# Kernel optimization log

Measured on AMD Instinct MI355X. Metric: run time of the kernel, lower is better.

The kernel has to match this reference:

```python
import jax, jax.numpy as jnp
import numpy as np

B, S, D, H, L, FF = 32, 512, 256, 8, 2, 512
E = 64  # embed_dim_per_feature
VOCABS = [20, 50, 100]
NCLS = 36
MAX_CONN, THR = 10, 0.6


def _ln(x, g, b, eps=1e-5):
    m = x.mean(-1, keepdims=True)
    v = ((x - m) ** 2).mean(-1, keepdims=True)
    return g * (x - m) / jnp.sqrt(v + eps) + b


def _build_adj(cat, cnt):
    # self loops + chain links + banded similarity links (create_mutation_graph_optimized)
    Bb, _, Ss = cat.shape
    adj = jnp.broadcast_to(jnp.eye(Ss, dtype=jnp.float32), (Bb, Ss, Ss))
    for d in range(1, MAX_CONN):
        if d >= Ss:
            break
        cat_sim = (cat[:, :, :-d] == cat[:, :, d:]).astype(jnp.float32).mean(1)
        cnt_sim = jnp.exp(-jnp.abs(cnt[:, :-d] - cnt[:, d:]) / 100.0)
        sim = 0.5 * (cat_sim + cnt_sim)  # [B, S-d]
        base = 1.0 if d == 1 else 0.0  # chain link stays 1 when sim<=thr
        val = jnp.where(sim > THR, sim, base)
        ii = jnp.arange(Ss - d)
        adj = adj.at[:, ii, ii + d].set(val)
        adj = adj.at[:, ii + d, ii].set(val)
    return adj


def setup_inputs():
    key = jax.random.key(0)
    ks = iter(jax.random.split(key, 40))
    def nrm(shape, s=0.02):
        return jax.random.normal(next(ks), shape, jnp.float32) * s
    return {
        "categorical_x": jax.random.randint(next(ks), (B, 3, S), 0, min(VOCABS)),
        "count_x": jax.random.uniform(next(ks), (B, S), jnp.float32) * 100.0,
        "emb0": nrm((VOCABS[0], E)), "emb1": nrm((VOCABS[1], E)), "emb2": nrm((VOCABS[2], E)),
        "cnt_W": nrm((1, E)), "cnt_b": jnp.zeros((E,), jnp.float32),
        "pos_enc": nrm((S, D)),
        "gat_W": nrm((L, D, D)), "gat_a": nrm((L, 2 * D, 1)),
        "qkv_W": nrm((L, 3 * D, D)), "qkv_b": jnp.zeros((L, 3 * D), jnp.float32),
        "outp_W": nrm((L, D, D)), "outp_b": jnp.zeros((L, D), jnp.float32),
        "ff1_W": nrm((L, FF, D)), "ff1_b": jnp.zeros((L, FF), jnp.float32),
        "ff2_W": nrm((L, D, FF)), "ff2_b": jnp.zeros((L, D), jnp.float32),
        "ln_g": jnp.ones((L, 3, D), jnp.float32), "ln_b": jnp.zeros((L, 3, D), jnp.float32),
        "cls1_W": nrm((D // 2, D)), "cls1_b": jnp.zeros((D // 2,), jnp.float32),
        "cls2_W": nrm((NCLS, D // 2)), "cls2_b": jnp.zeros((NCLS,), jnp.float32),
    }


def reference(categorical_x, count_x, emb0, emb1, emb2, cnt_W, cnt_b, pos_enc,
              gat_W, gat_a, qkv_W, qkv_b, outp_W, outp_b,
              ff1_W, ff1_b, ff2_W, ff2_b, ln_g, ln_b,
              cls1_W, cls1_b, cls2_W, cls2_b):
    Ss = categorical_x.shape[2]
    # per-timestep feature embedding + count projection, concat -> d_model
    x = jnp.concatenate([
        emb0[categorical_x[:, 0]], emb1[categorical_x[:, 1]], emb2[categorical_x[:, 2]],
        count_x[..., None] @ cnt_W + cnt_b], -1)
    x = x + pos_enc[:Ss]
    mask = _build_adj(categorical_x, count_x) > 0  # adj used only as mask
    dh = D // H
    for l in range(L):
        # GraphAttentionLayer: e_ij = Wh_i.a1 + Wh_j.a2 (same math as repeat+concat+matmul)
        Wh = x @ gat_W[l]
        e = (Wh @ gat_a[l][:D, 0])[:, :, None] + (Wh @ gat_a[l][D:, 0])[:, None, :]
        att = jax.nn.softmax(jnp.where(mask, e, -9e15), -1)
        g = jax.nn.elu(att @ Wh)
        x = _ln(x + g, ln_g[l, 0], ln_b[l, 0])
        # MultiheadAttention (batch_first, eval)
        qkv = x @ qkv_W[l].T + qkv_b[l]
        q, k, v = jnp.split(qkv, 3, -1)
        q = q.reshape(-1, Ss, H, dh)
        k = k.reshape(-1, Ss, H, dh)
        v = v.reshape(-1, Ss, H, dh)
        sc = jnp.einsum('bihd,bjhd->bhij', q, k) / jnp.sqrt(jnp.float32(dh))
        o = jnp.einsum('bhij,bjhd->bihd', jax.nn.softmax(sc, -1), v).reshape(-1, Ss, D)
        o = o @ outp_W[l].T + outp_b[l]
        x = _ln(x + o, ln_g[l, 1], ln_b[l, 1])
        # FFN
        ff = jax.nn.relu(x @ ff1_W[l].T + ff1_b[l]) @ ff2_W[l].T + ff2_b[l]
        x = _ln(x + ff, ln_g[l, 2], ln_b[l, 2])
    pooled = x.mean(1)
    h = jax.nn.relu(pooled @ cls1_W.T + cls1_b)
    return h @ cls2_W.T + cls2_b
```

## Files before the change

kernel.cpp:

```cpp
#include <hip/hip_runtime.h>
#include <hip/hip_bf16.h>
#include <math.h>

#define Bn 32
#define Sn 512
#define Dn 256
#define Hn 8
#define DHn 32
#define En 64
#define FFn 512
#define Ln 2
#define NCLSn 36
#define BANDR 9
#define NBn 19
#define Mn (Bn * Sn)

typedef __attribute__((ext_vector_type(8))) short s8v;
typedef __attribute__((ext_vector_type(4))) float f4v;
typedef __attribute__((ext_vector_type(4))) unsigned short us4;
typedef unsigned short ushortT;

__device__ __forceinline__ ushortT f2b(float f) {
    unsigned u = __float_as_uint(f);
    unsigned r = (u + 0x7FFFu + ((u >> 16) & 1u)) >> 16;
    return (ushortT)r;
}

#define GLDS16(g, l)                                                            \
    __builtin_amdgcn_global_load_lds(                                           \
        (const __attribute__((address_space(1))) void*)(g),                     \
        (__attribute__((address_space(3))) void*)(l), 16, 0, 0)

__global__ void k_f2b_all(const float* __restrict__ qkvW, const float* __restrict__ outpW,
                          const float* __restrict__ ff1W, const float* __restrict__ ff2W,
                          const float* __restrict__ gatW,
                          ushortT* __restrict__ qkvWb, ushortT* __restrict__ outpWb,
                          ushortT* __restrict__ ff1Wb, ushortT* __restrict__ ff2Wb,
                          ushortT* __restrict__ gatWb) {
    int bid = blockIdx.x;
    if (bid < 1024) {
        int i4 = bid * 256 + threadIdx.x;
        const float* src; ushortT* dst; int off;
        if (i4 < 98304)       { src = qkvW;  dst = qkvWb;  off = 0; }
        else if (i4 < 131072) { src = outpW; dst = outpWb; off = 98304; }
        else if (i4 < 196608) { src = ff1W;  dst = ff1Wb;  off = 131072; }
        else                  { src = ff2W;  dst = ff2Wb;  off = 196608; }
        int j = (i4 - off) * 4;
        float4 v = *(const float4*)(src + j);
        us4 o = {f2b(v.x), f2b(v.y), f2b(v.z), f2b(v.w)};
        *(us4*)(dst + j) = o;
    } else {
        int i = (bid - 1024) * 256 + threadIdx.x;
        int l = i >> 16, rem = i & 65535;
        int k = rem >> 8, n = rem & 255;
        gatWb[(l << 16) + n * 256 + k] = f2b(gatW[i]);
    }
}

__global__ void k_embed_mask(const int* __restrict__ cat, const float* __restrict__ cnt,
                             const float* __restrict__ e0, const float* __restrict__ e1,
                             const float* __restrict__ e2,
                             const float* __restrict__ cW, const float* __restrict__ cb,
                             const float* __restrict__ pos, float* __restrict__ x,
                             ushortT* __restrict__ xb, unsigned char* __restrict__ maskp) {
    if (blockIdx.x < Mn) {
        int bs = blockIdx.x;
        int d = threadIdx.x;
        int b = bs >> 9, s = bs & 511;
        float v;
        if (d < 64)       v = e0[cat[(b * 3 + 0) * Sn + s] * En + d];
        else if (d < 128) v = e1[cat[(b * 3 + 1) * Sn + s] * En + (d - 64)];
        else if (d < 192) v = e2[cat[(b * 3 + 2) * Sn + s] * En + (d - 128)];
        else              v = cnt[b * Sn + s] * cW[d - 192] + cb[d - 192];
        float y = v + pos[s * Dn + d];
        x[(size_t)bs * Dn + d] = y;
        xb[(size_t)bs * Dn + d] = f2b(y);
    } else {
        int idx = (blockIdx.x - Mn) * 256 + threadIdx.x;
        if (idx >= Bn * Sn * NBn) return;
        int off = idx % NBn;
        int bs = idx / NBn;
        int b = bs >> 9, i = bs & 511;
        int j = i + off - BANDR;
        unsigned char m = 0;
        if (j >= 0 && j < Sn) {
            int dd = off - BANDR;
            int ad = dd < 0 ? -dd : dd;
            if (ad <= 1) {
                m = 1;
            } else {
                int c = 0;
                for (int f = 0; f < 3; f++)
                    c += (cat[(b * 3 + f) * Sn + i] == cat[(b * 3 + f) * Sn + j]);
                float cat_sim = (float)c / 3.0f;
                float cnt_sim = expf(-fabsf(cnt[b * Sn + i] - cnt[b * Sn + j]) / 100.0f);
                float sim = 0.5f * (cat_sim + cnt_sim);
                m = (sim > 0.6f) ? 1 : 0;
            }
        }
        maskp[idx] = m;
    }
}

template <int ACT>
__global__ __launch_bounds__(256) void k_gemm_mfma(const ushortT* __restrict__ A,
                                                   const ushortT* __restrict__ Bt,
                                                   const float* __restrict__ bias,
                                                   ushortT* __restrict__ Cout,
                                                   int M, int N, int K) {
    __shared__ ushortT As[2][128 * 32];
    __shared__ ushortT Bs[2][128 * 32];
    int tid = threadIdx.x;
    int w = tid >> 6, lane = tid & 63;
    int g = lane >> 4, lr = lane & 15;
    int m0 = blockIdx.y * 128, n0 = blockIdx.x * 128;
    int wr = w >> 1, wc = w & 1;
    int NT = K >> 5;
    f4v acc[4][4];
#pragma unroll
    for (int m = 0; m < 4; m++)
#pragma unroll
        for (int n = 0; n < 4; n++) acc[m][n] = (f4v){0.f, 0.f, 0.f, 0.f};

    auto stage = [&](int t, int buf) {
        int k0 = t << 5;
#pragma unroll
        for (int r = 0; r < 2; r++) {
            int e = (tid + r * 256) * 8;
            int row = e >> 5, kk = e & 31;
            GLDS16(A + (size_t)(m0 + row) * K + k0 + kk, &As[buf][e]);
            GLDS16(Bt + (size_t)(n0 + row) * K + k0 + kk, &Bs[buf][e]);
        }
    };

    stage(0, 0);
    __syncthreads();
    for (int t = 0; t < NT; t++) {
        int cur = t & 1;
        if (t + 1 < NT) stage(t + 1, cur ^ 1);
        s8v af[4], bf[4];
#pragma unroll
        for (int m = 0; m < 4; m++)
            af[m] = *(const s8v*)(&As[cur][(wr * 64 + m * 16 + lr) * 32 + g * 8]);
#pragma unroll
        for (int n = 0; n < 4; n++)
            bf[n] = *(const s8v*)(&Bs[cur][(wc * 64 + n * 16 + lr) * 32 + g * 8]);
#pragma unroll
        for (int m = 0; m < 4; m++)
#pragma unroll
            for (int n = 0; n < 4; n++)
                acc[m][n] = __builtin_amdgcn_mfma_f32_16x16x32_bf16(af[m], bf[n], acc[m][n], 0, 0, 0);
        __syncthreads();
    }
#pragma unroll
    for (int m = 0; m < 4; m++) {
#pragma unroll
        for (int n = 0; n < 4; n++) {
            int col = n0 + wc * 64 + n * 16 + lr;
            float bv = bias ? bias[col] : 0.0f;
#pragma unroll
            for (int r = 0; r < 4; r++) {
                int row = m0 + wr * 64 + m * 16 + g * 4 + r;
                float v = acc[m][n][r] + bv;
                if (ACT == 1) v = fmaxf(v, 0.0f);
                Cout[(size_t)row * N + col] = f2b(v);
            }
        }
    }
}

template <int MODE>
__global__ __launch_bounds__(256) void k_gemm_row(const ushortT* __restrict__ A,
                                                  const ushortT* __restrict__ Bt,
                                                  const float* __restrict__ bias,
                                                  const float* __restrict__ ga,
                                                  float* __restrict__ a1h, float* __restrict__ a2h,
                                                  float* __restrict__ Whout,
                                                  const float* __restrict__ lg,
                                                  const float* __restrict__ lb,
                                                  float* __restrict__ x, ushortT* __restrict__ xb,
                                                  int K) {
    __shared__ ushortT As[2][32 * 32];
    __shared__ ushortT Bs[2][256 * 32];
    __shared__ float red1[32][4], red2[32][4];
    int tid = threadIdx.x;
    int w = tid >> 6, lane = tid & 63;
    int g = lane >> 4, lr = lane & 15;
    int m0 = blockIdx.x * 32;
    int NT = K >> 5;
    f4v acc[2][4];
#pragma unroll
    for (int m = 0; m < 2; m++)
#pragma unroll
        for (int n = 0; n < 4; n++) acc[m][n] = (f4v){0.f, 0.f, 0.f, 0.f};

    auto stage = [&](int t, int buf) {
        int k0 = t << 5;
        if (tid < 128) {
            int e = tid * 8;
            int row = e >> 5, kk = e & 31;
            GLDS16(A + (size_t)(m0 + row) * K + k0 + kk, &As[buf][e]);
        }
#pragma unroll
        for (int r = 0; r < 4; r++) {
            int e = (tid + r * 256) * 8;
            int row = e >> 5, kk = e & 31;
            GLDS16(Bt + (size_t)row * K + k0 + kk, &Bs[buf][e]);
        }
    };

    stage(0, 0);
    __syncthreads();
    for (int t = 0; t < NT; t++) {
        int cur = t & 1;
        if (t + 1 < NT) stage(t + 1, cur ^ 1);
        s8v af[2], bf[4];
#pragma unroll
        for (int m = 0; m < 2; m++)
            af[m] = *(const s8v*)(&As[cur][(m * 16 + lr) * 32 + g * 8]);
#pragma unroll
        for (int n = 0; n < 4; n++)
            bf[n] = *(const s8v*)(&Bs[cur][(w * 64 + n * 16 + lr) * 32 + g * 8]);
#pragma unroll
        for (int m = 0; m < 2; m++)
#pragma unroll
            for (int n = 0; n < 4; n++)
                acc[m][n] = __builtin_amdgcn_mfma_f32_16x16x32_bf16(af[m], bf[n], acc[m][n], 0, 0, 0);
        __syncthreads();
    }

    int cn[4];
#pragma unroll
    for (int n = 0; n < 4; n++) cn[n] = w * 64 + n * 16 + lr;

    if constexpr (MODE == 0) {
        float a1v[4], a2v[4];
#pragma unroll
        for (int n = 0; n < 4; n++) { a1v[n] = ga[cn[n]]; a2v[n] = ga[Dn + cn[n]]; }
#pragma unroll
        for (int m = 0; m < 2; m++)
#pragma unroll
            for (int r = 0; r < 4; r++) {
                int rowl = m * 16 + g * 4 + r;
                float p1 = 0.f, p2 = 0.f;
#pragma unroll
                for (int n = 0; n < 4; n++) {
                    float v = acc[m][n][r];
                    Whout[(size_t)(m0 + rowl) * Dn + cn[n]] = v;
                    p1 += v * a1v[n];
                    p2 += v * a2v[n];
                }
                p1 += __shfl_xor(p1, 1); p2 += __shfl_xor(p2, 1);
                p1 += __shfl_xor(p1, 2); p2 += __shfl_xor(p2, 2);
                p1 += __shfl_xor(p1, 4); p2 += __shfl_xor(p2, 4);
                p1 += __shfl_xor(p1, 8); p2 += __shfl_xor(p2, 8);
                if (lr == 0) { red1[rowl][w] = p1; red2[rowl][w] = p2; }
            }
        __syncthreads();
        if (tid < 32) {
            float t1 = red1[tid][0] + red1[tid][1] + red1[tid][2] + red1[tid][3];
            float t2 = red2[tid][0] + red2[tid][1] + red2[tid][2] + red2[tid][3];
            a1h[m0 + tid] = t1;
            a2h[m0 + tid] = t2;
        }
    } else {
        float bv[4], lgv[4], lbv[4];
#pragma unroll
        for (int n = 0; n < 4; n++) { bv[n] = bias[cn[n]]; lgv[n] = lg[cn[n]]; lbv[n] = lb[cn[n]]; }
#pragma unroll
        for (int m = 0; m < 2; m++)
#pragma unroll
            for (int r = 0; r < 4; r++) {
                int rowl = m * 16 + g * 4 + r;
                float s1 = 0.f, s2 = 0.f;
#pragma unroll
                for (int n = 0; n < 4; n++) {
                    float y = acc[m][n][r] + bv[n] + x[(size_t)(m0 + rowl) * Dn + cn[n]];
                    acc[m][n][r] = y;
                    s1 += y;
                    s2 += y * y;
                }
                s1 += __shfl_xor(s1, 1); s2 += __shfl_xor(s2, 1);
                s1 += __shfl_xor(s1, 2); s2 += __shfl_xor(s2, 2);
                s1 += __shfl_xor(s1, 4); s2 += __shfl_xor(s2, 4);
                s1 += __shfl_xor(s1, 8); s2 += __shfl_xor(s2, 8);
                if (lr == 0) { red1[rowl][w] = s1; red2[rowl][w] = s2; }
            }
        __syncthreads();
#pragma unroll
        for (int m = 0; m < 2; m++)
#pragma unroll
            for (int r = 0; r < 4; r++) {
                int rowl = m * 16 + g * 4 + r;
                float S1 = red1[rowl][0] + red1[rowl][1] + red1[rowl][2] + red1[rowl][3];
                float S2 = red2[rowl][0] + red2[rowl][1] + red2[rowl][2] + red2[rowl][3];
                float mean = S1 * (1.0f / Dn);
                float var = S2 * (1.0f / Dn) - mean * mean;
                float rs = rsqrtf(var + 1e-5f);
#pragma unroll
                for (int n = 0; n < 4; n++) {
                    float o = lgv[n] * (acc[m][n][r] - mean) * rs + lbv[n];
                    size_t idx = (size_t)(m0 + rowl) * Dn + cn[n];
                    x[idx] = o;
                    xb[idx] = f2b(o);
                }
            }
    }
}

__global__ __launch_bounds__(256) void k_gat_attn_ln(const float* __restrict__ Wh,
                                                     const float* __restrict__ a1h,
                                                     const float* __restrict__ a2h,
                                                     const unsigned char* __restrict__ mask,
                                                     const float* __restrict__ lg,
                                                     const float* __restrict__ lb,
                                                     float* __restrict__ x,
                                                     ushortT* __restrict__ xb) {
    int w = threadIdx.x >> 6, l = threadIdx.x & 63;
    int bs = blockIdx.x * 4 + w;
    int b = bs >> 9, i = bs & 511;
    float e = -1e30f;
    int j = i + l - BANDR;
    if (l < NBn && j >= 0 && j < Sn && mask[bs * NBn + l])
        e = a1h[bs] + a2h[(b << 9) + j];
    float mx = e;
#pragma unroll
    for (int o = 32; o; o >>= 1) mx = fmaxf(mx, __shfl_xor(mx, o));
    float p = (e > -1e29f) ? __expf(e - mx) : 0.0f;
    float sum = p;
#pragma unroll
    for (int o = 32; o; o >>= 1) sum += __shfl_xor(sum, o);
    p *= (1.0f / sum);
    int c4 = l * 4;
    const float* whb = Wh + (size_t)(b << 9) * Dn + c4;
    float gx = 0.f, gy = 0.f, gz = 0.f, gw = 0.f;
#pragma unroll
    for (int o = 0; o < NBn; o++) {
        float wo = __shfl(p, o);
        int jo = i + o - BANDR;
        jo = jo < 0 ? 0 : (jo > Sn - 1 ? Sn - 1 : jo);
        float4 v = *(const float4*)(whb + (size_t)jo * Dn);
        gx += wo * v.x; gy += wo * v.y; gz += wo * v.z; gw += wo * v.w;
    }
    gx = gx > 0.f ? gx : expm1f(gx);
    gy = gy > 0.f ? gy : expm1f(gy);
    gz = gz > 0.f ? gz : expm1f(gz);
    gw = gw > 0.f ? gw : expm1f(gw);
    float4 xv = *(const float4*)(x + (size_t)bs * Dn + c4);
    float y0 = xv.x + gx, y1 = xv.y + gy, y2 = xv.z + gz, y3 = xv.w + gw;
    float s1 = y0 + y1 + y2 + y3;
    float s2 = y0 * y0 + y1 * y1 + y2 * y2 + y3 * y3;
#pragma unroll
    for (int o = 32; o; o >>= 1) {
        s1 += __shfl_xor(s1, o);
        s2 += __shfl_xor(s2, o);
    }
    float mean = s1 * (1.0f / Dn);
    float var = s2 * (1.0f / Dn) - mean * mean;
    float r = rsqrtf(var + 1e-5f);
    float4 lgv = *(const float4*)(lg + c4);
    float4 lbv = *(const float4*)(lb + c4);
    float o0 = lgv.x * (y0 - mean) * r + lbv.x;
    float o1 = lgv.y * (y1 - mean) * r + lbv.y;
    float o2 = lgv.z * (y2 - mean) * r + lbv.z;
    float o3 = lgv.w * (y3 - mean) * r + lbv.w;
    *(float4*)(x + (size_t)bs * Dn + c4) = make_float4(o0, o1, o2, o3);
    us4 ob = {f2b(o0), f2b(o1), f2b(o2), f2b(o3)};
    *(us4*)(xb + (size_t)bs * Dn + c4) = ob;
}

__global__ __launch_bounds__(256) void k_attn_mfma(const ushortT* __restrict__ qkv,
                                                   ushortT* __restrict__ ob) {
    __shared__ ushortT Ks[2][64 * 32];
    __shared__ ushortT Vt[2][32 * 64];
    __shared__ ushortT Ps[4][2][16 * 72];
    int tid = threadIdx.x;
    int w = tid >> 6, lane = tid & 63;
    int g = lane >> 4, lr = lane & 15;
    int blk = blockIdx.x;
    int qh = blk & 1, h = (blk >> 1) & 7, b = blk >> 4;
    const ushortT* base = qkv + (size_t)b * Sn * 768;
    const ushortT* kbase = base + 256 + h * 32;
    const ushortT* vbase = base + 512 + h * 32;

    int krow2 = tid >> 3;
    int kc = (tid & 7) ^ (krow2 & 7);
    int kkv = krow2 * 2 + (kc >> 2);
    int kdd = (kc & 3) * 8;
    int vd0 = w * 8;

    int q0 = qh * 256 + w * 64;
    s8v qf[4];
#pragma unroll
    for (int m = 0; m < 4; m++)
        qf[m] = *(const s8v*)(base + (size_t)(q0 + m * 16 + lr) * 768 + h * 32 + g * 8);

    f4v o[4][2];
    float rl[4][4];
#pragma unroll
    for (int m = 0; m < 4; m++) {
        o[m][0] = (f4v){0.f, 0.f, 0.f, 0.f};
        o[m][1] = (f4v){0.f, 0.f, 0.f, 0.f};
#pragma unroll
        for (int r = 0; r < 4; r++) rl[m][r] = 0.f;
    }
    const float scale = 0.17677669529663687f;

    {
        GLDS16(kbase + (size_t)kkv * 768 + kdd, &Ks[0][tid * 8]);
        us4 v0 = *(const us4*)(vbase + (size_t)lane * 768 + vd0);
        us4 v1 = *(const us4*)(vbase + (size_t)lane * 768 + vd0 + 4);
#pragma unroll
        for (int jj = 0; jj < 4; jj++) {
            int d = vd0 + jj;
            Vt[0][d * 64 + (lane ^ ((d & 7) << 3))] = v0[jj];
            int d2 = d + 4;
            Vt[0][d2 * 64 + (lane ^ ((d2 & 7) << 3))] = v1[jj];
        }
    }
    __syncthreads();

    for (int kt = 0; kt < 8; kt++) {
        int cur = kt & 1, nxt = cur ^ 1;
        us4 v0, v1;
        if (kt < 7) {
            GLDS16(kbase + (size_t)((kt + 1) * 64 + kkv) * 768 + kdd, &Ks[nxt][tid * 8]);
            v0 = *(const us4*)(vbase + (size_t)((kt + 1) * 64 + lane) * 768 + vd0);
            v1 = *(const us4*)(vbase + (size_t)((kt + 1) * 64 + lane) * 768 + vd0 + 4);
        }
        s8v kf[4];
#pragma unroll
        for (int n = 0; n < 4; n++) {
            int row2 = n * 8 + (lr >> 1);
            int cc = (((lr & 1) << 2) + g) ^ (row2 & 7);
            kf[n] = *(const s8v*)(&Ks[cur][row2 * 64 + cc * 8]);
        }
        s8v vf[2][2];
#pragma unroll
        for (int cd = 0; cd < 2; cd++)
#pragma unroll
            for (int c2 = 0; c2 < 2; c2++) {
                int d = cd * 16 + lr;
                vf[cd][c2] = *(const s8v*)(&Vt[cur][d * 64 + ((c2 * 32 + g * 8) ^ ((d & 7) << 3))]);
            }
#pragma unroll
        for (int m = 0; m < 4; m++) {
            f4v s[4];
#pragma unroll
            for (int n = 0; n < 4; n++) {
                f4v z = (f4v){0.f, 0.f, 0.f, 0.f};
                s[n] = __builtin_amdgcn_mfma_f32_16x16x32_bf16(qf[m], kf[n], z, 0, 0, 0);
            }
            float pr[4][4];
#pragma unroll
            for (int r = 0; r < 4; r++) {
                pr[0][r] = __expf(fminf(s[0][r] * scale, 60.f));
                pr[1][r] = __expf(fminf(s[1][r] * scale, 60.f));
                pr[2][r] = __expf(fminf(s[2][r] * scale, 60.f));
                pr[3][r] = __expf(fminf(s[3][r] * scale, 60.f));
                rl[m][r] += (pr[0][r] + pr[1][r]) + (pr[2][r] + pr[3][r]);
            }
            if (m > 0) {
                int pb = (m - 1) & 1;
                s8v pf0 = *(const s8v*)(&Ps[w][pb][lr * 72 + g * 8]);
                s8v pf1 = *(const s8v*)(&Ps[w][pb][lr * 72 + 32 + g * 8]);
                o[m - 1][0] = __builtin_amdgcn_mfma_f32_16x16x32_bf16(pf0, vf[0][0], o[m - 1][0], 0, 0, 0);
                o[m - 1][0] = __builtin_amdgcn_mfma_f32_16x16x32_bf16(pf1, vf[0][1], o[m - 1][0], 0, 0, 0);
                o[m - 1][1] = __builtin_amdgcn_mfma_f32_16x16x32_bf16(pf0, vf[1][0], o[m - 1][1], 0, 0, 0);
                o[m - 1][1] = __builtin_amdgcn_mfma_f32_16x16x32_bf16(pf1, vf[1][1], o[m - 1][1], 0, 0, 0);
            }
            int sb = m & 1;
#pragma unroll
            for (int r = 0; r < 4; r++) {
                int rr = g * 4 + r;
                Ps[w][sb][rr * 72 + lr]      = f2b(pr[0][r]);
                Ps[w][sb][rr * 72 + 16 + lr] = f2b(pr[1][r]);
                Ps[w][sb][rr * 72 + 32 + lr] = f2b(pr[2][r]);
                Ps[w][sb][rr * 72 + 48 + lr] = f2b(pr[3][r]);
            }
        }
        {
            s8v pf0 = *(const s8v*)(&Ps[w][1][lr * 72 + g * 8]);
            s8v pf1 = *(const s8v*)(&Ps[w][1][lr * 72 + 32 + g * 8]);
            o[3][0] = __builtin_amdgcn_mfma_f32_16x16x32_bf16(pf0, vf[0][0], o[3][0], 0, 0, 0);
            o[3][0] = __builtin_amdgcn_mfma_f32_16x16x32_bf16(pf1, vf[0][1], o[3][0], 0, 0, 0);
            o[3][1] = __builtin_amdgcn_mfma_f32_16x16x32_bf16(pf0, vf[1][0], o[3][1], 0, 0, 0);
            o[3][1] = __builtin_amdgcn_mfma_f32_16x16x32_bf16(pf1, vf[1][1], o[3][1], 0, 0, 0);
        }
        if (kt < 7) {
#pragma unroll
            for (int jj = 0; jj < 4; jj++) {
                int d = vd0 + jj;
                Vt[nxt][d * 64 + (lane ^ ((d & 7) << 3))] = v0[jj];
                int d2 = d + 4;
                Vt[nxt][d2 * 64 + (lane ^ ((d2 & 7) << 3))] = v1[jj];
            }
        }
        __syncthreads();
    }
#pragma unroll
    for (int m = 0; m < 4; m++) {
#pragma unroll
        for (int r = 0; r < 4; r++) {
            float t = rl[m][r];
            t += __shfl_xor(t, 1);
            t += __shfl_xor(t, 2);
            t += __shfl_xor(t, 4);
            t += __shfl_xor(t, 8);
            float inv = 1.0f / t;
            int qr = q0 + m * 16 + g * 4 + r;
            size_t obase = ((size_t)(b * Sn + qr)) * Dn + h * 32;
            ob[obase + lr] = f2b(o[m][0][r] * inv);
            ob[obase + 16 + lr] = f2b(o[m][1][r] * inv);
        }
    }
}

__global__ void k_pool_cls(const float* __restrict__ x, const float* __restrict__ w1,
                           const float* __restrict__ b1, const float* __restrict__ w2,
                           const float* __restrict__ b2, float* __restrict__ out) {
    int b = blockIdx.x;
    int t = threadIdx.x;
    __shared__ float pooled[Dn];
    __shared__ float hbuf[128];
    float s = 0.f;
    const float* xp = x + (size_t)(b << 9) * Dn + t;
    for (int sx = 0; sx < Sn; sx++) s += xp[(size_t)sx * Dn];
    pooled[t] = s * (1.0f / Sn);
    __syncthreads();
    if (t < 128) {
        float a = b1[t];
        for (int k = 0; k < Dn; k++) a += pooled[k] * w1[t * Dn + k];
        hbuf[t] = fmaxf(a, 0.0f);
    }
    __syncthreads();
    if (t < NCLSn) {
        float a2 = b2[t];
        for (int k = 0; k < 128; k++) a2 += hbuf[k] * w2[t * 128 + k];
        out[b * NCLSn + t] = a2;
    }
}

extern "C" void kernel_launch(void* const* d_in, const int* in_sizes, int n_in,
                              void* d_out, int out_size, void* d_ws, size_t ws_size,
                              hipStream_t stream) {
    const int* cat = (const int*)d_in[0];
    const float* cnt = (const float*)d_in[1];
    const float* emb0 = (const float*)d_in[2];
    const float* emb1 = (const float*)d_in[3];
    const float* emb2 = (const float*)d_in[4];
    const float* cnt_W = (const float*)d_in[5];
    const float* cnt_b = (const float*)d_in[6];
    const float* pos_enc = (const float*)d_in[7];
    const float* gat_W = (const float*)d_in[8];
    const float* gat_a = (const float*)d_in[9];
    const float* qkv_W = (const float*)d_in[10];
    const float* qkv_b = (const float*)d_in[11];
    const float* outp_W = (const float*)d_in[12];
    const float* outp_b = (const float*)d_in[13];
    const float* ff1_W = (const float*)d_in[14];
    const float* ff1_b = (const float*)d_in[15];
    const float* ff2_W = (const float*)d_in[16];
    const float* ff2_b = (const float*)d_in[17];
    const float* ln_g = (const float*)d_in[18];
    const float* ln_b = (const float*)d_in[19];
    const float* cls1_W = (const float*)d_in[20];
    const float* cls1_b = (const float*)d_in[21];
    const float* cls2_W = (const float*)d_in[22];
    const float* cls2_b = (const float*)d_in[23];
    float* out = (float*)d_out;

    char* wp = (char*)d_ws;
    float* x = (float*)wp;        wp += (size_t)Mn * Dn * 4;
    float* tmpf = (float*)wp;     wp += (size_t)Mn * Dn * 4;
    ushortT* xb = (ushortT*)wp;   wp += (size_t)Mn * Dn * 2;
    ushortT* qkvb = (ushortT*)wp; wp += (size_t)Mn * 3 * Dn * 2;
    ushortT* ffb = qkvb;
    ushortT* obb = (ushortT*)wp;  wp += (size_t)Mn * Dn * 2;
    float* a1h = (float*)wp;      wp += (size_t)Mn * 4;
    float* a2h = (float*)wp;      wp += (size_t)Mn * 4;
    unsigned char* mask = (unsigned char*)wp; wp += (size_t)Mn * NBn;
    ushortT* gatWb = (ushortT*)wp;  wp += (size_t)Ln * Dn * Dn * 2;
    ushortT* qkvWb = (ushortT*)wp;  wp += (size_t)Ln * 3 * Dn * Dn * 2;
    ushortT* outpWb = (ushortT*)wp; wp += (size_t)Ln * Dn * Dn * 2;
    ushortT* ff1Wb = (ushortT*)wp;  wp += (size_t)Ln * FFn * Dn * 2;
    ushortT* ff2Wb = (ushortT*)wp;  wp += (size_t)Ln * Dn * FFn * 2;

    k_f2b_all<<<1536, 256, 0, stream>>>(qkv_W, outp_W, ff1_W, ff2_W, gat_W,
                                        qkvWb, outpWb, ff1Wb, ff2Wb, gatWb);
    k_embed_mask<<<Mn + 1216, 256, 0, stream>>>(cat, cnt, emb0, emb1, emb2, cnt_W, cnt_b,
                                                pos_enc, x, xb, mask);

    for (int l = 0; l < Ln; l++) {
        k_gemm_row<0><<<Mn / 32, 256, 0, stream>>>(
            xb, gatWb + (size_t)l * Dn * Dn, nullptr,
            gat_a + (size_t)l * 2 * Dn, a1h, a2h, tmpf,
            nullptr, nullptr, nullptr, nullptr, Dn);
        k_gat_attn_ln<<<Mn / 4, 256, 0, stream>>>(tmpf, a1h, a2h, mask,
                                                  ln_g + (l * 3 + 0) * Dn, ln_b + (l * 3 + 0) * Dn, x, xb);
        k_gemm_mfma<0><<<dim3(3 * Dn / 128, Mn / 128), 256, 0, stream>>>(
            xb, qkvWb + (size_t)l * 3 * Dn * Dn, qkv_b + l * 3 * Dn, qkvb, Mn, 3 * Dn, Dn);
        k_attn_mfma<<<Bn * Hn * 2, 256, 0, stream>>>(qkvb, obb);
        k_gemm_row<1><<<Mn / 32, 256, 0, stream>>>(
            obb, outpWb + (size_t)l * Dn * Dn, outp_b + l * Dn,
            nullptr, nullptr, nullptr, nullptr,
            ln_g + (l * 3 + 1) * Dn, ln_b + (l * 3 + 1) * Dn, x, xb, Dn);
        k_gemm_mfma<1><<<dim3(FFn / 128, Mn / 128), 256, 0, stream>>>(
            xb, ff1Wb + (size_t)l * FFn * Dn, ff1_b + l * FFn, ffb, Mn, FFn, Dn);
        k_gemm_row<1><<<Mn / 32, 256, 0, stream>>>(
            ffb, ff2Wb + (size_t)l * Dn * FFn, ff2_b + l * Dn,
            nullptr, nullptr, nullptr, nullptr,
            ln_g + (l * 3 + 2) * Dn, ln_b + (l * 3 + 2) * Dn, x, xb, FFn);
    }

    k_pool_cls<<<Bn, 256, 0, stream>>>(x, cls1_W, cls1_b, cls2_W, cls2_b, out);
}
```

Baseline: 314.8 us.

## Split attention queries into quarters and single-buffer K/V shared tiles

The attention kernel now launches four blocks per (batch, head), each handling 128 queries with 32 per wave instead of 64. This doubles the grid to raise occupancy and parallelism. The K/V shared-memory tiles drop from double to single buffering: fragments are read into registers, a barrier follows, and then the next tile is loaded, which cuts LDS use. The trade-off is that every block reloads the full K/V, doubling K/V global traffic, and the extra barrier each iteration reduces load/compute overlap.

Measured after the change: 318.3 us. About the same (+1.1%).

```diff
diff --git a/kernel.cpp b/kernel.cpp
--- a/kernel.cpp
+++ b/kernel.cpp
@@ -371,14 +371,14 @@
 
 __global__ __launch_bounds__(256) void k_attn_mfma(const ushortT* __restrict__ qkv,
                                                    ushortT* __restrict__ ob) {
-    __shared__ ushortT Ks[2][64 * 32];
-    __shared__ ushortT Vt[2][32 * 64];
+    __shared__ ushortT Ks[64 * 32];
+    __shared__ ushortT Vt[32 * 64];
     __shared__ ushortT Ps[4][2][16 * 72];
     int tid = threadIdx.x;
     int w = tid >> 6, lane = tid & 63;
     int g = lane >> 4, lr = lane & 15;
     int blk = blockIdx.x;
-    int qh = blk & 1, h = (blk >> 1) & 7, b = blk >> 4;
+    int qq = blk & 3, h = (blk >> 2) & 7, b = blk >> 5;
     const ushortT* base = qkv + (size_t)b * Sn * 768;
     const ushortT* kbase = base + 256 + h * 32;
     const ushortT* vbase = base + 512 + h * 32;
@@ -389,16 +389,16 @@
     int kdd = (kc & 3) * 8;
     int vd0 = w * 8;
 
-    int q0 = qh * 256 + w * 64;
-    s8v qf[4];
-#pragma unroll
-    for (int m = 0; m < 4; m++)
+    int q0 = qq * 128 + w * 32;
+    s8v qf[2];
+#pragma unroll
+    for (int m = 0; m < 2; m++)
         qf[m] = *(const s8v*)(base + (size_t)(q0 + m * 16 + lr) * 768 + h * 32 + g * 8);
 
-    f4v o[4][2];
-    float rl[4][4];
-#pragma unroll
-    for (int m = 0; m < 4; m++) {
+    f4v o[2][2];
+    float rl[2][4];
+#pragma unroll
+    for (int m = 0; m < 2; m++) {
         o[m][0] = (f4v){0.f, 0.f, 0.f, 0.f};
         o[m][1] = (f4v){0.f, 0.f, 0.f, 0.f};
 #pragma unroll
@@ -407,33 +407,26 @@
     const float scale = 0.17677669529663687f;
 
     {
-        GLDS16(kbase + (size_t)kkv * 768 + kdd, &Ks[0][tid * 8]);
+        GLDS16(kbase + (size_t)kkv * 768 + kdd, &Ks[tid * 8]);
         us4 v0 = *(const us4*)(vbase + (size_t)lane * 768 + vd0);
         us4 v1 = *(const us4*)(vbase + (size_t)lane * 768 + vd0 + 4);
 #pragma unroll
         for (int jj = 0; jj < 4; jj++) {
             int d = vd0 + jj;
-            Vt[0][d * 64 + (lane ^ ((d & 7) << 3))] = v0[jj];
+            Vt[d * 64 + (lane ^ ((d & 7) << 3))] = v0[jj];
             int d2 = d + 4;
-            Vt[0][d2 * 64 + (lane ^ ((d2 & 7) << 3))] = v1[jj];
+            Vt[d2 * 64 + (lane ^ ((d2 & 7) << 3))] = v1[jj];
         }
     }
     __syncthreads();
 
     for (int kt = 0; kt < 8; kt++) {
-        int cur = kt & 1, nxt = cur ^ 1;
-        us4 v0, v1;
-        if (kt < 7) {
-            GLDS16(kbase + (size_t)((kt + 1) * 64 + kkv) * 768 + kdd, &Ks[nxt][tid * 8]);
-            v0 = *(const us4*)(vbase + (size_t)((kt + 1) * 64 + lane) * 768 + vd0);
-            v1 = *(const us4*)(vbase + (size_t)((kt + 1) * 64 + lane) * 768 + vd0 + 4);
-        }
         s8v kf[4];
 #pragma unroll
         for (int n = 0; n < 4; n++) {
             int row2 = n * 8 + (lr >> 1);
             int cc = (((lr & 1) << 2) + g) ^ (row2 & 7);
-            kf[n] = *(const s8v*)(&Ks[cur][row2 * 64 + cc * 8]);
+            kf[n] = *(const s8v*)(&Ks[row2 * 64 + cc * 8]);
         }
         s8v vf[2][2];
 #pragma unroll
@@ -441,10 +434,17 @@
 #pragma unroll
             for (int c2 = 0; c2 < 2; c2++) {
                 int d = cd * 16 + lr;
-                vf[cd][c2] = *(const s8v*)(&Vt[cur][d * 64 + ((c2 * 32 + g * 8) ^ ((d & 7) << 3))]);
-            }
-#pragma unroll
-        for (int m = 0; m < 4; m++) {
+                vf[cd][c2] = *(const s8v*)(&Vt[d * 64 + ((c2 * 32 + g * 8) ^ ((d & 7) << 3))]);
+            }
+        __syncthreads();
+        us4 v0, v1;
+        if (kt < 7) {
+            GLDS16(kbase + (size_t)((kt + 1) * 64 + kkv) * 768 + kdd, &Ks[tid * 8]);
+            v0 = *(const us4*)(vbase + (size_t)((kt + 1) * 64 + lane) * 768 + vd0);
+            v1 = *(const us4*)(vbase + (size_t)((kt + 1) * 64 + lane) * 768 + vd0 + 4);
+        }
+#pragma unroll
+        for (int m = 0; m < 2; m++) {
             f4v s[4];
 #pragma unroll
             for (int n = 0; n < 4; n++) {
@@ -461,13 +461,12 @@
                 rl[m][r] += (pr[0][r] + pr[1][r]) + (pr[2][r] + pr[3][r]);
             }
             if (m > 0) {
-                int pb = (m - 1) & 1;
-                s8v pf0 = *(const s8v*)(&Ps[w][pb][lr * 72 + g * 8]);
-                s8v pf1 = *(const s8v*)(&Ps[w][pb][lr * 72 + 32 + g * 8]);
-                o[m - 1][0] = __builtin_amdgcn_mfma_f32_16x16x32_bf16(pf0, vf[0][0], o[m - 1][0], 0, 0, 0);
-                o[m - 1][0] = __builtin_amdgcn_mfma_f32_16x16x32_bf16(pf1, vf[0][1], o[m - 1][0], 0, 0, 0);
-                o[m - 1][1] = __builtin_amdgcn_mfma_f32_16x16x32_bf16(pf0, vf[1][0], o[m - 1][1], 0, 0, 0);
-                o[m - 1][1] = __builtin_amdgcn_mfma_f32_16x16x32_bf16(pf1, vf[1][1], o[m - 1][1], 0, 0, 0);
+                s8v pf0 = *(const s8v*)(&Ps[w][0][lr * 72 + g * 8]);
+                s8v pf1 = *(const s8v*)(&Ps[w][0][lr * 72 + 32 + g * 8]);
+                o[0][0] = __builtin_amdgcn_mfma_f32_16x16x32_bf16(pf0, vf[0][0], o[0][0], 0, 0, 0);
+                o[0][0] = __builtin_amdgcn_mfma_f32_16x16x32_bf16(pf1, vf[0][1], o[0][0], 0, 0, 0);
+                o[0][1] = __builtin_amdgcn_mfma_f32_16x16x32_bf16(pf0, vf[1][0], o[0][1], 0, 0, 0);
+                o[0][1] = __builtin_amdgcn_mfma_f32_16x16x32_bf16(pf1, vf[1][1], o[0][1], 0, 0, 0);
             }
             int sb = m & 1;
 #pragma unroll
@@ -482,24 +481,24 @@
         {
             s8v pf0 = *(const s8v*)(&Ps[w][1][lr * 72 + g * 8]);
             s8v pf1 = *(const s8v*)(&Ps[w][1][lr * 72 + 32 + g * 8]);
-            o[3][0] = __builtin_amdgcn_mfma_f32_16x16x32_bf16(pf0, vf[0][0], o[3][0], 0, 0, 0);
-            o[3][0] = __builtin_amdgcn_mfma_f32_16x16x32_bf16(pf1, vf[0][1], o[3][0], 0, 0, 0);
-            o[3][1] = __builtin_amdgcn_mfma_f32_16x16x32_bf16(pf0, vf[1][0], o[3][1], 0, 0, 0);
-            o[3][1] = __builtin_amdgcn_mfma_f32_16x16x32_bf16(pf1, vf[1][1], o[3][1], 0, 0, 0);
+            o[1][0] = __builtin_amdgcn_mfma_f32_16x16x32_bf16(pf0, vf[0][0], o[1][0], 0, 0, 0);
+            o[1][0] = __builtin_amdgcn_mfma_f32_16x16x32_bf16(pf1, vf[0][1], o[1][0], 0, 0, 0);
+            o[1][1] = __builtin_amdgcn_mfma_f32_16x16x32_bf16(pf0, vf[1][0], o[1][1], 0, 0, 0);
+            o[1][1] = __builtin_amdgcn_mfma_f32_16x16x32_bf16(pf1, vf[1][1], o[1][1], 0, 0, 0);
         }
         if (kt < 7) {
 #pragma unroll
             for (int jj = 0; jj < 4; jj++) {
                 int d = vd0 + jj;
-                Vt[nxt][d * 64 + (lane ^ ((d & 7) << 3))] = v0[jj];
+                Vt[d * 64 + (lane ^ ((d & 7) << 3))] = v0[jj];
                 int d2 = d + 4;
-                Vt[nxt][d2 * 64 + (lane ^ ((d2 & 7) << 3))] = v1[jj];
+                Vt[d2 * 64 + (lane ^ ((d2 & 7) << 3))] = v1[jj];
             }
         }
         __syncthreads();
     }
 #pragma unroll
-    for (int m = 0; m < 4; m++) {
+    for (int m = 0; m < 2; m++) {
 #pragma unroll
         for (int r = 0; r < 4; r++) {
             float t = rl[m][r];
@@ -600,7 +599,7 @@
                                                   ln_g + (l * 3 + 0) * Dn, ln_b + (l * 3 + 0) * Dn, x, xb);
         k_gemm_mfma<0><<<dim3(3 * Dn / 128, Mn / 128), 256, 0, stream>>>(
             xb, qkvWb + (size_t)l * 3 * Dn * Dn, qkv_b + l * 3 * Dn, qkvb, Mn, 3 * Dn, Dn);
-        k_attn_mfma<<<Bn * Hn * 2, 256, 0, stream>>>(qkvb, obb);
+        k_attn_mfma<<<Bn * Hn * 4, 256, 0, stream>>>(qkvb, obb);
         k_gemm_row<1><<<Mn / 32, 256, 0, stream>>>(
             obb, outpWb + (size_t)l * Dn * Dn, outp_b + l * Dn,
             nullptr, nullptr, nullptr, nullptr,
```
